# Kernel optimization log

Measured on AMD Instinct MI355X. Metric: run time of the kernel, lower is better.

## Reference

```python
import jax, jax.numpy as jnp
import numpy as np
from jax import lax

EPS = 1e-20
DN = ('NCHW', 'OIHW', 'NCHW')


def nconv(x, c, w, b, pad):
    """Normalized convolution (Eldesokey NConv2d): conv(data*conf)/conv(conf)."""
    pads = [(pad, pad), (pad, pad)]
    denom = lax.conv_general_dilated(c, w, (1, 1), pads, dimension_numbers=DN)
    nomin = lax.conv_general_dilated(x * c, w, (1, 1), pads, dimension_numbers=DN)
    out = nomin / (denom + EPS) + b[None, :, None, None]
    s = jnp.sum(w, axis=(1, 2, 3))  # per-out-channel kernel sum
    cout = denom / s[None, :, None, None]
    return out, cout


def pool_gather(x, c):
    """2x2 stride-2 max-pool on c; gather x at the argmax locations (vectorized
    replacement for the per-(batch,channel) Python-loop unpool gather)."""
    B, C, H, W = c.shape
    cw = c.reshape(B, C, H // 2, 2, W // 2, 2).transpose(0, 1, 2, 4, 3, 5).reshape(B, C, H // 2, W // 2, 4)
    xw = x.reshape(B, C, H // 2, 2, W // 2, 2).transpose(0, 1, 2, 4, 3, 5).reshape(B, C, H // 2, W // 2, 4)
    idx = jnp.argmax(cw, axis=-1)[..., None]
    c_ds = jnp.take_along_axis(cw, idx, axis=-1)[..., 0]
    x_ds = jnp.take_along_axis(xw, idx, axis=-1)[..., 0]
    return x_ds, c_ds / 4.0


def up2(a):
    """Nearest-neighbor 2x upsample (exact-doubling case of F.interpolate)."""
    return jnp.repeat(jnp.repeat(a, 2, axis=2), 2, axis=3)


def setup_inputs() -> dict:
    key = jax.random.key(0)
    ks = jax.random.split(key, 16)
    C = 32  # (input_channels-1) * mid_channels = 1 * 32
    u = lambda k, sh: jax.random.uniform(k, sh, dtype=jnp.float32) * 0.05
    z = lambda k, sh: jax.random.normal(k, sh, dtype=jnp.float32) * 0.01
    return {
        'x': jax.random.uniform(ks[0], (2, 2, 512, 512), dtype=jnp.float32),
        'w1': u(ks[1], (C, 1, 5, 5)), 'b1': z(ks[2], (C,)),
        'w2': u(ks[3], (C, C, 5, 5)), 'b2': z(ks[4], (C,)),
        'w3': u(ks[5], (C, C, 5, 5)), 'b3': z(ks[6], (C,)),
        'w4': u(ks[7], (C, 2 * C, 3, 3)), 'b4': z(ks[8], (C,)),
        'w5': u(ks[9], (C, 2 * C, 3, 3)), 'b5': z(ks[10], (C,)),
        'w6': u(ks[11], (C, 2 * C, 3, 3)), 'b6': z(ks[12], (C,)),
        'w7': u(ks[13], (1, C, 1, 1)), 'b7': z(ks[14], (1,)),
    }


def reference(x, w1, b1, w2, b2, w3, b3, w4, b4, w5, b5, w6, b6, w7, b7):
    cat = lambda a, b: jnp.concatenate((a, b), axis=1)
    x0 = x[:, 0:1]                                 # data channel
    c0 = jnp.broadcast_to(x[:, 1:2], x0.shape)     # confidence channel repeated
    x1, c1 = nconv(x0, c0, w1, b1, 2)
    x1, c1 = nconv(x1, c1, w2, b2, 2)
    x1, c1 = nconv(x1, c1, w3, b3, 2)
    x1_ds, c1_ds = pool_gather(x1, c1)
    x2_ds, c2_ds = nconv(x1_ds, c1_ds, w2, b2, 2)  # nconv2 weight reuse (as in source)
    x2_ds, c2_ds = nconv(x2_ds, c2_ds, w3, b3, 2)
    x2_dss, c2_dss = pool_gather(x2_ds, c2_ds)
    x3_ds, c3_ds = nconv(x2_dss, c2_dss, w2, b2, 2)
    x3_dss, c3_dss = pool_gather(x3_ds, c3_ds)
    x4_ds, c4_ds = nconv(x3_dss, c3_dss, w2, b2, 2)
    x4, c4 = up2(x4_ds), up2(c4_ds)
    x34_ds, c34_ds = nconv(cat(x3_ds, x4), cat(c3_ds, c4), w4, b4, 1)
    x34, c34 = up2(x34_ds), up2(c34_ds)
    x23_ds, c23_ds = nconv(cat(x2_ds, x34), cat(c2_ds, c34), w5, b5, 1)
    x23, c23 = up2(x23_ds), up2(c23_ds)
    xout, cout = nconv(cat(x23, x1), cat(c23, c1), w6, b6, 1)
    xout, cout = nconv(xout, cout, w7, b7, 0)
    return xout
```

## Files before the change

### kernel.cpp

```cpp
#include <hip/hip_runtime.h>
#include <hip/hip_bf16.h>

#define EPSF 1e-20f

using short8  = __attribute__((ext_vector_type(8))) short;
using float4f = __attribute__((ext_vector_type(4))) float;

__device__ __forceinline__ unsigned short f2bf(float f) {
    __hip_bfloat16 h = __float2bfloat16(f);
    return __builtin_bit_cast(unsigned short, h);
}
__device__ __forceinline__ float bf2f(unsigned short u) {
    __hip_bfloat16 h = __builtin_bit_cast(__hip_bfloat16, u);
    return __bfloat162float(h);
}
__device__ __forceinline__ float frcp(float x) { return __builtin_amdgcn_rcpf(x); }

__global__ void wprep_k(const float* __restrict__ w1, const float* __restrict__ w2,
                        const float* __restrict__ w3, const float* __restrict__ w4,
                        const float* __restrict__ w5, const float* __restrict__ w6,
                        float* __restrict__ wt1,
                        float* __restrict__ is1, float* __restrict__ is2,
                        float* __restrict__ is3, float* __restrict__ is4,
                        float* __restrict__ is5, float* __restrict__ is6,
                        unsigned short* __restrict__ wf2, unsigned short* __restrict__ wf3,
                        unsigned short* __restrict__ wf4, unsigned short* __restrict__ wf5,
                        unsigned short* __restrict__ wf6) {
    const int tid = threadIdx.x;
    if (blockIdx.x >= 420) {
        int wid = (blockIdx.x - 420) * 4 + (tid >> 6);
        if (wid >= 192) return;
        int task = wid >> 5, co = wid & 31, lane = tid & 63;
        const float* w; int n; float* s;
        switch (task) {
            case 0: w = w1; n = 25;  s = is1; break;
            case 1: w = w2; n = 800; s = is2; break;
            case 2: w = w3; n = 800; s = is3; break;
            case 3: w = w4; n = 576; s = is4; break;
            case 4: w = w5; n = 576; s = is5; break;
            default: w = w6; n = 576; s = is6; break;
        }
        float acc = 0.f;
        for (int i = lane; i < n; i += 64) acc += w[co * n + i];
#pragma unroll
        for (int off = 1; off < 64; off <<= 1) acc += __shfl_xor(acc, off);
        if (lane == 0) s[co] = 1.0f / acc;
        return;
    }
    int idx = blockIdx.x * 256 + tid;
    if (idx < 800) {
        int co = idx / 25, t = idx % 25;
        wt1[t * 32 + co] = w1[idx];
        return;
    }
    if (idx < 992) return;
    int r = idx - 992;
    const float* w; unsigned short* wf; int CIN, KK, cxor;
    if (r < 25600)        {             w = w2; wf = wf2; CIN = 32; KK = 25; cxor = 0;  }
    else if (r < 51200)   { r -= 25600; w = w3; wf = wf3; CIN = 32; KK = 25; cxor = 0;  }
    else if (r < 69632)   { r -= 51200; w = w4; wf = wf4; CIN = 64; KK = 9;  cxor = 0;  }
    else if (r < 88064)   { r -= 69632; w = w5; wf = wf5; CIN = 64; KK = 9;  cxor = 0;  }
    else if (r < 106496)  { r -= 88064; w = w6; wf = wf6; CIN = 64; KK = 9;  cxor = 32; }
    else return;
    int j = r & 7, lane = (r >> 3) & 63, cot = (r >> 9) & 1, ks = r >> 10;
    int phase = ks / KK, tap = ks - phase * KK;
    int co = cot * 16 + (lane & 15);
    int ci = (phase * 32 + (lane >> 4) * 8 + j) ^ cxor;
    wf[r] = f2bf(w[((long)co * CIN + ci) * KK + tap]);
}

__global__ __launch_bounds__(256)
void conv1_k(const float* __restrict__ x, const float* __restrict__ wt,
             const float* __restrict__ bias, const float* __restrict__ is_,
             unsigned short* __restrict__ out, int H, int W) {
    constexpr int TIW = 36, TIH = 12, TSZ = TIW * TIH;
    __shared__ float sc[TSZ], sp[TSZ];
    const int tid = threadIdx.x;
    const int tx = tid & 31, ty = tid >> 5;
    const int ox0 = blockIdx.x * 32, oy0 = blockIdx.y * 8, b = blockIdx.z;
    const long HW = (long)H * W;
    const float* xd = x + (long)(b * 2) * HW;
    const float* xc = xd + HW;

    for (int i = tid; i < TSZ; i += 256) {
        int py = i / TIW, px = i - py * TIW;
        int gy = oy0 - 2 + py, gx = ox0 - 2 + px;
        float c = 0.f, d = 0.f;
        if (gy >= 0 && gy < H && gx >= 0 && gx < W) {
            long g = (long)gy * W + gx;
            c = xc[g]; d = xd[g];
        }
        sc[i] = c;
        sp[i] = d * c;
    }
    __syncthreads();

    float ac[32], ap[32];
#pragma unroll
    for (int i = 0; i < 32; ++i) { ac[i] = 0.f; ap[i] = 0.f; }
#pragma unroll
    for (int dy = 0; dy < 5; ++dy) {
#pragma unroll
        for (int dx = 0; dx < 5; ++dx) {
            const int li = (ty + dy) * TIW + tx + dx;
            float cf = sc[li];
            float pv = sp[li];
            const float* wr = wt + (dy * 5 + dx) * 32;
#pragma unroll
            for (int co = 0; co < 32; ++co) {
                ac[co] = fmaf(wr[co], cf, ac[co]);
                ap[co] = fmaf(wr[co], pv, ap[co]);
            }
        }
    }

    const int xx = ox0 + tx, yy = oy0 + ty;
    unsigned short* po = out + ((long)(b * 2 + 0) * HW + (long)yy * W + xx) * 32;
    unsigned short* co_ = out + ((long)(b * 2 + 1) * HW + (long)yy * W + xx) * 32;
#pragma unroll
    for (int g = 0; g < 4; ++g) {
        uint4 vp, vc;
        unsigned int pw[4], cw[4];
#pragma unroll
        for (int h = 0; h < 4; ++h) {
            int c0 = g * 8 + h * 2, c1 = c0 + 1;
            float d0 = ac[c0], d1 = ac[c1];
            float ox0v = fmaf(ap[c0], frcp(d0 + EPSF), bias[c0]);
            float ox1v = fmaf(ap[c1], frcp(d1 + EPSF), bias[c1]);
            float oc0 = d0 * is_[c0], oc1 = d1 * is_[c1];
            pw[h] = (unsigned int)f2bf(ox0v * oc0) | ((unsigned int)f2bf(ox1v * oc1) << 16);
            cw[h] = (unsigned int)f2bf(oc0) | ((unsigned int)f2bf(oc1) << 16);
        }
        vp.x = pw[0]; vp.y = pw[1]; vp.z = pw[2]; vp.w = pw[3];
        vc.x = cw[0]; vc.y = cw[1]; vc.z = cw[2]; vc.w = cw[3];
        *(uint4*)(po + g * 8) = vp;
        *(uint4*)(co_ + g * 8) = vc;
    }
}

template <int KS, int NPH, bool FUSE7>
__global__ __launch_bounds__(512, 4)
void mconv_k(const unsigned short* __restrict__ s1,
             const unsigned short* __restrict__ s2,
             const unsigned short* __restrict__ wf,
             const float* __restrict__ bias, const float* __restrict__ sden,
             unsigned short* __restrict__ out, float* __restrict__ xout,
             const float* __restrict__ w7, const float* __restrict__ b7,
             int H, int W) {
    constexpr int R = KS / 2, KK = KS * KS;
    constexpr int TIH = 16 + KS - 1, TIW = 16 + KS - 1;
    constexpr int RT = TIW & 3;
    constexpr int PCS = TIH * TIW * 32;
    constexpr int NCH = TIH * TIW * 4;
    __shared__ unsigned short lds[2 * PCS];

    const int tid = threadIdx.x;
    const int wv = tid >> 6, lane = tid & 63, n = lane & 15, q = lane >> 4;
    const int ox0 = blockIdx.x * 16, oy0 = blockIdx.y * 16, b = blockIdx.z;
    const long HW = (long)H * W;

    float4f accP[2][2], accC[2][2];
#pragma unroll
    for (int mt = 0; mt < 2; ++mt)
#pragma unroll
        for (int ct = 0; ct < 2; ++ct) {
            accP[mt][ct] = (float4f)0.f;
            accC[mt][ct] = (float4f)0.f;
        }

    int so4[4];
#pragma unroll
    for (int j = 0; j < 4; ++j) so4[j] = ((q + n + j) & 3) * 8;
    const int PB = (2 * wv) * TIW + n;

    for (int ph = 0; ph < NPH; ++ph) {
        const unsigned short* src = (NPH == 2 && ph == 1) ? s2 : s1;
        if (ph) __syncthreads();
        for (int it = 0; it < (2 * NCH + 511) / 512; ++it) {
            int ch = it * 512 + tid;
            if (ch < 2 * NCH) {
                int pc = ch / NCH, c2 = ch - pc * NCH;
                int pix = c2 >> 2, k8 = c2 & 3;
                int py = pix / TIW, px = pix - py * TIW;
                int gy = oy0 - R + py, gx = ox0 - R + px;
                uint4 v = make_uint4(0, 0, 0, 0);
                if (gy >= 0 && gy < H && gx >= 0 && gx < W) {
                    long gi;
                    if (NPH == 2 && ph == 1)
                        gi = ((long)(b * 2 + pc) * (HW >> 2) +
                              (long)(gy >> 1) * (W >> 1) + (gx >> 1)) * 32 + k8 * 8;
                    else
                        gi = ((long)(b * 2 + pc) * HW + (long)gy * W + gx) * 32 + k8 * 8;
                    v = *(const uint4*)(src + gi);
                }
                *(uint4*)(lds + pc * PCS + pix * 32 + ((k8 + pix) & 3) * 8) = v;
            }
        }
        __syncthreads();
#pragma unroll
        for (int dy = 0; dy < KS; ++dy) {
#pragma unroll
            for (int dx = 0; dx < KS; ++dx) {
                const int ks = ph * KK + dy * KS + dx;
                short8 a0 = ((const short8*)wf)[(ks * 2 + 0) * 64 + lane];
                short8 a1 = ((const short8*)wf)[(ks * 2 + 1) * 64 + lane];
#pragma unroll
                for (int mt = 0; mt < 2; ++mt) {
                    const int p = PB + (mt + dy) * TIW + dx;
                    const int off = p * 32 + so4[(dx + RT * (mt + dy) / 2 * 2) & 3];
                    short8 bp = *(const short8*)(lds + off);
                    short8 bc = *(const short8*)(lds + off + PCS);
                    accP[mt][0] = __builtin_amdgcn_mfma_f32_16x16x32_bf16(a0, bp, accP[mt][0], 0, 0, 0);
                    accP[mt][1] = __builtin_amdgcn_mfma_f32_16x16x32_bf16(a1, bp, accP[mt][1], 0, 0, 0);
                    accC[mt][0] = __builtin_amdgcn_mfma_f32_16x16x32_bf16(a0, bc, accC[mt][0], 0, 0, 0);
                    accC[mt][1] = __builtin_amdgcn_mfma_f32_16x16x32_bf16(a1, bc, accC[mt][1], 0, 0, 0);
                }
            }
        }
    }

    float4f b4[2], s4[2];
    b4[0] = *(const float4f*)(bias + q * 4);
    b4[1] = *(const float4f*)(bias + 16 + q * 4);
    s4[0] = *(const float4f*)(sden + q * 4);
    s4[1] = *(const float4f*)(sden + 16 + q * 4);

    if (!FUSE7) {
#pragma unroll
        for (int pl = 0; pl < 2; ++pl) {
            __syncthreads();
#pragma unroll
            for (int mt = 0; mt < 2; ++mt) {
                const int pix = (2 * wv + mt) * 16 + n;
#pragma unroll
                for (int ct = 0; ct < 2; ++ct) {
                    unsigned int w0, w1;
                    if (pl == 0) {
                        float d0 = accC[mt][ct][0], d1 = accC[mt][ct][1];
                        float d2 = accC[mt][ct][2], d3 = accC[mt][ct][3];
                        float x0 = fmaf(accP[mt][ct][0], frcp(d0 + EPSF), b4[ct][0]) * (d0 * s4[ct][0]);
                        float x1 = fmaf(accP[mt][ct][1], frcp(d1 + EPSF), b4[ct][1]) * (d1 * s4[ct][1]);
                        float x2 = fmaf(accP[mt][ct][2], frcp(d2 + EPSF), b4[ct][2]) * (d2 * s4[ct][2]);
                        float x3 = fmaf(accP[mt][ct][3], frcp(d3 + EPSF), b4[ct][3]) * (d3 * s4[ct][3]);
                        w0 = (unsigned int)f2bf(x0) | ((unsigned int)f2bf(x1) << 16);
                        w1 = (unsigned int)f2bf(x2) | ((unsigned int)f2bf(x3) << 16);
                    } else {
                        float c0 = accC[mt][ct][0] * s4[ct][0], c1 = accC[mt][ct][1] * s4[ct][1];
                        float c2 = accC[mt][ct][2] * s4[ct][2], c3 = accC[mt][ct][3] * s4[ct][3];
                        w0 = (unsigned int)f2bf(c0) | ((unsigned int)f2bf(c1) << 16);
                        w1 = (unsigned int)f2bf(c2) | ((unsigned int)f2bf(c3) << 16);
                    }
                    uint2 v; v.x = w0; v.y = w1;
                    *(uint2*)(lds + pix * 32 + ((ct * 2 + (q >> 1) + n) & 3) * 8 + (q & 1) * 4) = v;
                }
            }
            __syncthreads();
            const unsigned short* obase = out + (long)(b * 2 + pl) * HW * 32;
#pragma unroll
            for (int it = 0; it < 2; ++it) {
                int off = it * 512 + tid;
                int pix = off >> 2, sub = off & 3;
                uint4 v = *(const uint4*)(lds + pix * 32 + ((sub + pix) & 3) * 8);
                int ry = pix >> 4, rx = pix & 15;
                *(uint4*)(obase + ((long)(oy0 + ry) * W + ox0 + rx) * 32 + sub * 8) = v;
            }
        }
    } else {
        float4f w74[2];
        w74[0] = *(const float4f*)(w7 + q * 4);
        w74[1] = *(const float4f*)(w7 + 16 + q * 4);
        const float b7v = b7[0];
#pragma unroll
        for (int mt = 0; mt < 2; ++mt) {
            float num = 0.f, den = 0.f;
#pragma unroll
            for (int ct = 0; ct < 2; ++ct)
#pragma unroll
                for (int r = 0; r < 4; ++r) {
                    float d = accC[mt][ct][r];
                    float oxv = fmaf(accP[mt][ct][r], frcp(d + EPSF), b4[ct][r]);
                    float oc = d * s4[ct][r];
                    num = fmaf(w74[ct][r], oxv * oc, num);
                    den = fmaf(w74[ct][r], oc, den);
                }
            num += __shfl_xor(num, 16); num += __shfl_xor(num, 32);
            den += __shfl_xor(den, 16); den += __shfl_xor(den, 32);
            if (q == 0) {
                const int oy = oy0 + 2 * wv + mt;
                const int ox = ox0 + n;
                xout[(long)b * HW + (long)oy * W + ox] = fmaf(num, frcp(den + EPSF), b7v);
            }
        }
    }
}

__global__ void pool_k(const unsigned short* __restrict__ in, unsigned short* __restrict__ out,
                       int H2, int W2, int total) {
    int idx = blockIdx.x * 256 + threadIdx.x;
    if (idx >= total) return;
    int k8 = idx & 3, t = idx >> 2;
    long HW2 = (long)H2 * W2;
    int pix2 = (int)(t % HW2), b = (int)(t / HW2);
    int h = pix2 / W2, w = pix2 - h * W2;
    int W = W2 * 2;
    long HW = HW2 * 4;
    long p00 = ((long)(2 * h) * W + 2 * w) * 32 + k8 * 8;
    const unsigned short* pin = in + (long)(b * 2 + 0) * HW * 32;
    const unsigned short* cin = in + (long)(b * 2 + 1) * HW * 32;
    union U { uint4 v; unsigned short s[8]; };
    U c0, c1, c2, c3, p0, p1, p2, p3, rp, rc;
    c0.v = *(const uint4*)(cin + p00);             c1.v = *(const uint4*)(cin + p00 + 32);
    c2.v = *(const uint4*)(cin + p00 + (long)W * 32); c3.v = *(const uint4*)(cin + p00 + (long)W * 32 + 32);
    p0.v = *(const uint4*)(pin + p00);             p1.v = *(const uint4*)(pin + p00 + 32);
    p2.v = *(const uint4*)(pin + p00 + (long)W * 32); p3.v = *(const uint4*)(pin + p00 + (long)W * 32 + 32);
#pragma unroll
    for (int e = 0; e < 8; ++e) {
        float cv = bf2f(c0.s[e]), pv = bf2f(p0.s[e]);
        float c01 = bf2f(c1.s[e]); if (c01 > cv) { cv = c01; pv = bf2f(p1.s[e]); }
        float c10 = bf2f(c2.s[e]); if (c10 > cv) { cv = c10; pv = bf2f(p2.s[e]); }
        float c11 = bf2f(c3.s[e]); if (c11 > cv) { cv = c11; pv = bf2f(p3.s[e]); }
        rp.s[e] = f2bf(pv * 0.25f);
        rc.s[e] = f2bf(cv * 0.25f);
    }
    long ob = ((long)pix2) * 32 + k8 * 8;
    *(uint4*)(out + (long)(b * 2 + 0) * HW2 * 32 + ob) = rp.v;
    *(uint4*)(out + (long)(b * 2 + 1) * HW2 * 32 + ob) = rc.v;
}

extern "C" void kernel_launch(void* const* d_in, const int* in_sizes, int n_in,
                              void* d_out, int out_size, void* d_ws, size_t ws_size,
                              hipStream_t stream) {
    const float* x  = (const float*)d_in[0];
    const float* w1 = (const float*)d_in[1];
    const float* b1 = (const float*)d_in[2];
    const float* w2 = (const float*)d_in[3];
    const float* b2 = (const float*)d_in[4];
    const float* w3 = (const float*)d_in[5];
    const float* b3 = (const float*)d_in[6];
    const float* w4 = (const float*)d_in[7];
    const float* b4 = (const float*)d_in[8];
    const float* w5 = (const float*)d_in[9];
    const float* b5 = (const float*)d_in[10];
    const float* w6 = (const float*)d_in[11];
    const float* b6 = (const float*)d_in[12];
    const float* w7 = (const float*)d_in[13];
    const float* b7 = (const float*)d_in[14];

    const size_t HW1 = 512 * 512, HW2s = 256 * 256, HW3s = 128 * 128, HW4s = 64 * 64;

    const size_t WARENA = 400000;
    float* fa = (float*)d_ws;
    float *wt1 = fa;
    float *s1 = wt1 + 800, *s2 = s1 + 32, *s3 = s2 + 32;
    float *s4 = s3 + 32, *s5 = s4 + 32, *s6 = s5 + 32;
    unsigned short* ua = (unsigned short*)((char*)d_ws + 4096);
    unsigned short *wf2 = ua;
    unsigned short *wf3 = wf2 + 25600;
    unsigned short *wf4 = wf3 + 25600;
    unsigned short *wf5 = wf4 + 18432;
    unsigned short *wf6 = wf5 + 18432;
    unsigned short* buf = (unsigned short*)((char*)d_ws + WARENA);

    const size_t E1 = 2 * 2 * HW1 * 32;
    const size_t E2 = 2 * 2 * HW2s * 32, E3 = 2 * 2 * HW3s * 32, E4 = 2 * 2 * HW4s * 32;
    unsigned short* A = buf;
    unsigned short* B = A + E1;
    unsigned short* P = B;
    unsigned short* Q = P + E2;
    unsigned short* S = Q + E2;
    unsigned short* T = S + E3;
    unsigned short* U = T + E3;
    unsigned short* V = U + E4;

    if (ws_size < WARENA + 2 * E1 * sizeof(unsigned short)) return;

    wprep_k<<<468, 256, 0, stream>>>(w1, w2, w3, w4, w5, w6,
                                     wt1, s1, s2, s3, s4, s5, s6,
                                     wf2, wf3, wf4, wf5, wf6);

    dim3 blk(256), blkm(512);
    dim3 g1c(16, 64, 2);
    dim3 g1(32, 32, 2), g2(16, 16, 2), g3(8, 8, 2), g4(4, 4, 2);

    conv1_k<<<g1c, blk, 0, stream>>>(x, wt1, b1, s1, A, 512, 512);
    mconv_k<5, 1, false><<<g1, blkm, 0, stream>>>(A, nullptr, wf2, b2, s2, B, nullptr, nullptr, nullptr, 512, 512);
    mconv_k<5, 1, false><<<g1, blkm, 0, stream>>>(B, nullptr, wf3, b3, s3, A, nullptr, nullptr, nullptr, 512, 512);

    pool_k<<<(int)((2 * HW2s * 4 + 255) / 256), blk, 0, stream>>>(A, P, 256, 256, (int)(2 * HW2s * 4));
    mconv_k<5, 1, false><<<g2, blkm, 0, stream>>>(P, nullptr, wf2, b2, s2, Q, nullptr, nullptr, nullptr, 256, 256);
    mconv_k<5, 1, false><<<g2, blkm, 0, stream>>>(Q, nullptr, wf3, b3, s3, P, nullptr, nullptr, nullptr, 256, 256);

    pool_k<<<(int)((2 * HW3s * 4 + 255) / 256), blk, 0, stream>>>(P, S, 128, 128, (int)(2 * HW3s * 4));
    mconv_k<5, 1, false><<<g3, blkm, 0, stream>>>(S, nullptr, wf2, b2, s2, T, nullptr, nullptr, nullptr, 128, 128);

    pool_k<<<(int)((2 * HW4s * 4 + 255) / 256), blk, 0, stream>>>(T, U, 64, 64, (int)(2 * HW4s * 4));
    mconv_k<5, 1, false><<<g4, blkm, 0, stream>>>(U, nullptr, wf2, b2, s2, V, nullptr, nullptr, nullptr, 64, 64);

    mconv_k<3, 2, false><<<g3, blkm, 0, stream>>>(T, V, wf4, b4, s4, S, nullptr, nullptr, nullptr, 128, 128);
    mconv_k<3, 2, false><<<g2, blkm, 0, stream>>>(P, S, wf5, b5, s5, Q, nullptr, nullptr, nullptr, 256, 256);
    mconv_k<3, 2, true><<<g1, blkm, 0, stream>>>(A, Q, wf6, b6, s6, nullptr, (float*)d_out, w7, b7, 512, 512);
}
```

Measured before the change: 405.9 us.

## Fuse 2x2 confidence max-pool into conv epilogue and tweak LDS swizzle

Removes the three standalone pool_k launches. The conv kernels that feed a pooling stage now compute the pooled data/confidence pair directly from their fp32 accumulators, using lane shuffles across neighbouring columns and the two rows each wave already owns, and write the quarter-size output. This avoids re-reading the full-resolution bf16 activations from global memory and saves the kernel launches. It also adds an extra term to the LDS store/load swizzle, likely to cut bank conflicts. Pooling on unrounded fp32 values can pick a different argmax than before on near-ties.

Result: faster. 392.9 us (-3.2%).

```diff
diff --git a/kernel.cpp b/kernel.cpp
--- a/kernel.cpp
+++ b/kernel.cpp
@@ -138,7 +138,7 @@
     }
 }
 
-template <int KS, int NPH, bool FUSE7>
+template <int KS, int NPH, bool FUSE7, bool POOL>
 __global__ __launch_bounds__(512, 4)
 void mconv_k(const unsigned short* __restrict__ s1,
              const unsigned short* __restrict__ s2,
@@ -146,6 +146,7 @@
              const float* __restrict__ bias, const float* __restrict__ sden,
              unsigned short* __restrict__ out, float* __restrict__ xout,
              const float* __restrict__ w7, const float* __restrict__ b7,
+             unsigned short* __restrict__ pout,
              int H, int W) {
     constexpr int R = KS / 2, KK = KS * KS;
     constexpr int TIH = 16 + KS - 1, TIW = 16 + KS - 1;
@@ -226,6 +227,43 @@
     s4[1] = *(const float4f*)(sden + 16 + q * 4);
 
     if (!FUSE7) {
+        if (POOL) {
+            const int W2 = W >> 1;
+            const long HW4 = HW >> 2;
+#pragma unroll
+            for (int ct = 0; ct < 2; ++ct) {
+                unsigned int pw[2], cw[2];
+                unsigned short ps[4], cs[4];
+#pragma unroll
+                for (int r = 0; r < 4; ++r) {
+                    float d0 = accC[0][ct][r], d1 = accC[1][ct][r];
+                    float c00 = d0 * s4[ct][r];
+                    float c10 = d1 * s4[ct][r];
+                    float p00 = fmaf(accP[0][ct][r], frcp(d0 + EPSF), b4[ct][r]) * c00;
+                    float p10 = fmaf(accP[1][ct][r], frcp(d1 + EPSF), b4[ct][r]) * c10;
+                    float c01 = __shfl_xor(c00, 1), c11 = __shfl_xor(c10, 1);
+                    float p01 = __shfl_xor(p00, 1), p11 = __shfl_xor(p10, 1);
+                    float bc = c00, bp = p00;
+                    if (c01 > bc) { bc = c01; bp = p01; }
+                    if (c10 > bc) { bc = c10; bp = p10; }
+                    if (c11 > bc) { bc = c11; bp = p11; }
+                    ps[r] = f2bf(bp * 0.25f);
+                    cs[r] = f2bf(bc * 0.25f);
+                }
+                if (!(n & 1)) {
+                    pw[0] = (unsigned int)ps[0] | ((unsigned int)ps[1] << 16);
+                    pw[1] = (unsigned int)ps[2] | ((unsigned int)ps[3] << 16);
+                    cw[0] = (unsigned int)cs[0] | ((unsigned int)cs[1] << 16);
+                    cw[1] = (unsigned int)cs[2] | ((unsigned int)cs[3] << 16);
+                    int gy2 = (oy0 >> 1) + wv, gx2 = (ox0 >> 1) + (n >> 1);
+                    long pb = ((long)gy2 * W2 + gx2) * 32 + ct * 16 + q * 4;
+                    uint2 vp; vp.x = pw[0]; vp.y = pw[1];
+                    uint2 vc; vc.x = cw[0]; vc.y = cw[1];
+                    *(uint2*)(pout + (long)(b * 2 + 0) * HW4 * 32 + pb) = vp;
+                    *(uint2*)(pout + (long)(b * 2 + 1) * HW4 * 32 + pb) = vc;
+                }
+            }
+        }
 #pragma unroll
         for (int pl = 0; pl < 2; ++pl) {
             __syncthreads();
@@ -251,7 +289,8 @@
                         w1 = (unsigned int)f2bf(c2) | ((unsigned int)f2bf(c3) << 16);
                     }
                     uint2 v; v.x = w0; v.y = w1;
-                    *(uint2*)(lds + pix * 32 + ((ct * 2 + (q >> 1) + n) & 3) * 8 + (q & 1) * 4) = v;
+                    *(uint2*)(lds + pix * 32 +
+                              ((ct * 2 + (q >> 1) + n + (n >> 2)) & 3) * 8 + (q & 1) * 4) = v;
                 }
             }
             __syncthreads();
@@ -260,7 +299,7 @@
             for (int it = 0; it < 2; ++it) {
                 int off = it * 512 + tid;
                 int pix = off >> 2, sub = off & 3;
-                uint4 v = *(const uint4*)(lds + pix * 32 + ((sub + pix) & 3) * 8);
+                uint4 v = *(const uint4*)(lds + pix * 32 + ((sub + pix + (pix >> 2)) & 3) * 8);
                 int ry = pix >> 4, rx = pix & 15;
                 *(uint4*)(obase + ((long)(oy0 + ry) * W + ox0 + rx) * 32 + sub * 8) = v;
             }
@@ -292,39 +331,6 @@
             }
         }
     }
-}
-
-__global__ void pool_k(const unsigned short* __restrict__ in, unsigned short* __restrict__ out,
-                       int H2, int W2, int total) {
-    int idx = blockIdx.x * 256 + threadIdx.x;
-    if (idx >= total) return;
-    int k8 = idx & 3, t = idx >> 2;
-    long HW2 = (long)H2 * W2;
-    int pix2 = (int)(t % HW2), b = (int)(t / HW2);
-    int h = pix2 / W2, w = pix2 - h * W2;
-    int W = W2 * 2;
-    long HW = HW2 * 4;
-    long p00 = ((long)(2 * h) * W + 2 * w) * 32 + k8 * 8;
-    const unsigned short* pin = in + (long)(b * 2 + 0) * HW * 32;
-    const unsigned short* cin = in + (long)(b * 2 + 1) * HW * 32;
-    union U { uint4 v; unsigned short s[8]; };
-    U c0, c1, c2, c3, p0, p1, p2, p3, rp, rc;
-    c0.v = *(const uint4*)(cin + p00);             c1.v = *(const uint4*)(cin + p00 + 32);
-    c2.v = *(const uint4*)(cin + p00 + (long)W * 32); c3.v = *(const uint4*)(cin + p00 + (long)W * 32 + 32);
-    p0.v = *(const uint4*)(pin + p00);             p1.v = *(const uint4*)(pin + p00 + 32);
-    p2.v = *(const uint4*)(pin + p00 + (long)W * 32); p3.v = *(const uint4*)(pin + p00 + (long)W * 32 + 32);
-#pragma unroll
-    for (int e = 0; e < 8; ++e) {
-        float cv = bf2f(c0.s[e]), pv = bf2f(p0.s[e]);
-        float c01 = bf2f(c1.s[e]); if (c01 > cv) { cv = c01; pv = bf2f(p1.s[e]); }
-        float c10 = bf2f(c2.s[e]); if (c10 > cv) { cv = c10; pv = bf2f(p2.s[e]); }
-        float c11 = bf2f(c3.s[e]); if (c11 > cv) { cv = c11; pv = bf2f(p3.s[e]); }
-        rp.s[e] = f2bf(pv * 0.25f);
-        rc.s[e] = f2bf(cv * 0.25f);
-    }
-    long ob = ((long)pix2) * 32 + k8 * 8;
-    *(uint4*)(out + (long)(b * 2 + 0) * HW2 * 32 + ob) = rp.v;
-    *(uint4*)(out + (long)(b * 2 + 1) * HW2 * 32 + ob) = rc.v;
 }
 
 extern "C" void kernel_launch(void* const* d_in, const int* in_sizes, int n_in,
@@ -383,20 +389,17 @@
     dim3 g1(32, 32, 2), g2(16, 16, 2), g3(8, 8, 2), g4(4, 4, 2);
 
     conv1_k<<<g1c, blk, 0, stream>>>(x, wt1, b1, s1, A, 512, 512);
-    mconv_k<5, 1, false><<<g1, blkm, 0, stream>>>(A, nullptr, wf2, b2, s2, B, nullptr, nullptr, nullptr, 512, 512);
-    mconv_k<5, 1, false><<<g1, blkm, 0, stream>>>(B, nullptr, wf3, b3, s3, A, nullptr, nullptr, nullptr, 512, 512);
-
-    pool_k<<<(int)((2 * HW2s * 4 + 255) / 256), blk, 0, stream>>>(A, P, 256, 256, (int)(2 * HW2s * 4));
-    mconv_k<5, 1, false><<<g2, blkm, 0, stream>>>(P, nullptr, wf2, b2, s2, Q, nullptr, nullptr, nullptr, 256, 256);
-    mconv_k<5, 1, false><<<g2, blkm, 0, stream>>>(Q, nullptr, wf3, b3, s3, P, nullptr, nullptr, nullptr, 256, 256);
-
-    pool_k<<<(int)((2 * HW3s * 4 + 255) / 256), blk, 0, stream>>>(P, S, 128, 128, (int)(2 * HW3s * 4));
-    mconv_k<5, 1, false><<<g3, blkm, 0, stream>>>(S, nullptr, wf2, b2, s2, T, nullptr, nullptr, nullptr, 128, 128);
-
-    pool_k<<<(int)((2 * HW4s * 4 + 255) / 256), blk, 0, stream>>>(T, U, 64, 64, (int)(2 * HW4s * 4));
-    mconv_k<5, 1, false><<<g4, blkm, 0, stream>>>(U, nullptr, wf2, b2, s2, V, nullptr, nullptr, nullptr, 64, 64);
-
-    mconv_k<3, 2, false><<<g3, blkm, 0, stream>>>(T, V, wf4, b4, s4, S, nullptr, nullptr, nullptr, 128, 128);
-    mconv_k<3, 2, false><<<g2, blkm, 0, stream>>>(P, S, wf5, b5, s5, Q, nullptr, nullptr, nullptr, 256, 256);
-    mconv_k<3, 2, true><<<g1, blkm, 0, stream>>>(A, Q, wf6, b6, s6, nullptr, (float*)d_out, w7, b7, 512, 512);
-}
+    mconv_k<5, 1, false, false><<<g1, blkm, 0, stream>>>(A, nullptr, wf2, b2, s2, B, nullptr, nullptr, nullptr, nullptr, 512, 512);
+    mconv_k<5, 1, false, true><<<g1, blkm, 0, stream>>>(B, nullptr, wf3, b3, s3, A, nullptr, nullptr, nullptr, P, 512, 512);
+
+    mconv_k<5, 1, false, false><<<g2, blkm, 0, stream>>>(P, nullptr, wf2, b2, s2, Q, nullptr, nullptr, nullptr, nullptr, 256, 256);
+    mconv_k<5, 1, false, true><<<g2, blkm, 0, stream>>>(Q, nullptr, wf3, b3, s3, P, nullptr, nullptr, nullptr, S, 256, 256);
+
+    mconv_k<5, 1, false, true><<<g3, blkm, 0, stream>>>(S, nullptr, wf2, b2, s2, T, nullptr, nullptr, nullptr, U, 128, 128);
+
+    mconv_k<5, 1, false, false><<<g4, blkm, 0, stream>>>(U, nullptr, wf2, b2, s2, V, nullptr, nullptr, nullptr, nullptr, 64, 64);
+
+    mconv_k<3, 2, false, false><<<g3, blkm, 0, stream>>>(T, V, wf4, b4, s4, S, nullptr, nullptr, nullptr, nullptr, 128, 128);
+    mconv_k<3, 2, false, false><<<g2, blkm, 0, stream>>>(P, S, wf5, b5, s5, Q, nullptr, nullptr, nullptr, nullptr, 256, 256);
+    mconv_k<3, 2, true, false><<<g1, blkm, 0, stream>>>(A, Q, wf6, b6, s6, nullptr, (float*)d_out, w7, b7, nullptr, 512, 512);
+}
```
